# Kernel tuning notes

Hardware: AMD Instinct MI355X
Metric: run time of the kernel (lower is better)

## Reference

```python
import jax, jax.numpy as jnp
import numpy as np
import math

IN_DIM = 1024
INTER_DIM = 1024
HIDDEN_DIM = 1024
OUT_DIM = 1024
NUM_GROUPS = 16
N = 8192
EPS = 1e-5


def setup_inputs() -> dict:
    key = jax.random.key(0)
    ks = jax.random.split(key, 20)
    def lin(kw, kb, fan_out, fan_in):
        bound = 1.0 / math.sqrt(fan_in)
        W = jax.random.uniform(kw, (fan_out, fan_in), jnp.float32, -bound, bound)
        b = jax.random.uniform(kb, (fan_out,), jnp.float32, -bound, bound)
        return W, b
    Wq, bq = lin(ks[0], ks[1], INTER_DIM, IN_DIM)
    Wk, bk = lin(ks[2], ks[3], INTER_DIM, IN_DIM)
    Wv, bv = lin(ks[4], ks[5], INTER_DIM, IN_DIM)
    Wr, br = lin(ks[6], ks[7], HIDDEN_DIM, INTER_DIM)
    Wc, bc = lin(ks[8], ks[9], HIDDEN_DIM, OUT_DIM)
    Wp, bp = lin(ks[10], ks[11], OUT_DIM, 2 * HIDDEN_DIM)
    return {
        'h': jax.random.normal(ks[12], (N, IN_DIM), jnp.float32),
        'D': jax.random.uniform(ks[13], (N, N), jnp.float32),
        'h_prime': jax.random.normal(ks[14], (N, OUT_DIM), jnp.float32),
        'Wq': Wq, 'bq': bq, 'Wk': Wk, 'bk': bk, 'Wv': Wv, 'bv': bv,
        'Wr': Wr, 'br': br, 'Wc': Wc, 'bc': bc, 'Wp': Wp, 'bp': bp,
        'prelu_w': jnp.full((OUT_DIM,), 0.25, jnp.float32),
        'gn_w': jnp.ones((OUT_DIM,), jnp.float32),
        'gn_b': jnp.zeros((OUT_DIM,), jnp.float32),
    }


def reference(h, D, h_prime, Wq, bq, Wk, bk, Wv, bv, Wr, br, Wc, bc, Wp, bp, prelu_w, gn_w, gn_b):
    # projections [N, inter]
    Q = h @ Wq.T + bq
    K = h @ Wk.T + bk
    V = h @ Wv.T + bv
    # decay-masked retention: softmax(D * QK^T / sqrt(d)) @ V
    scores = (Q @ K.T) * (1.0 / math.sqrt(INTER_DIM))   # [N, N]
    attn = jax.nn.softmax(D * scores, axis=-1)
    h_ret = attn @ V                                     # [N, inter]
    h_ret = jax.nn.gelu(h_ret @ Wr.T + br, approximate=False)  # [N, hidden]
    h_cat = h_prime @ Wc.T + bc                          # [N, hidden]
    combined = jnp.concatenate([h_ret, h_cat], axis=-1)  # [N, 2*hidden]
    x = combined @ Wp.T + bp                             # [N, out]
    # PReLU (per-channel slope over feature dim)
    x = jnp.where(x >= 0, x, prelu_w[None, :] * x)
    # GroupNorm over (C, N) layout: normalize each group of channels jointly over all N
    xt = x.T                                             # [C, N]
    xg = xt.reshape(NUM_GROUPS, -1)                      # [G, (C/G)*N]
    mean = jnp.mean(xg, axis=1, keepdims=True)
    var = jnp.var(xg, axis=1, keepdims=True)
    xg = (xg - mean) * jax.lax.rsqrt(var + EPS)
    xt = xg.reshape(OUT_DIM, N) * gn_w[:, None] + gn_b[:, None]
    return xt.T                                          # [N, out]
```

## Files before the change

kernel.cpp:

```cpp
#include <hip/hip_runtime.h>
#include <hip/hip_bf16.h>


typedef __bf16 bf16x8 __attribute__((ext_vector_type(8)));
typedef float f32x4 __attribute__((ext_vector_type(4)));
typedef unsigned short ushort_t;
typedef unsigned short ushort8 __attribute__((ext_vector_type(8)));


__device__ __forceinline__ void gload_lds16(const void* g, void* lds) {
  __builtin_amdgcn_global_load_lds((const __attribute__((address_space(1))) void*)g,
                                   (__attribute__((address_space(3))) void*)lds,
                                   16, 0, 0);
}

__device__ __forceinline__ ushort_t f2bu(float x) {
  __hip_bfloat16 h = __float2bfloat16(x);
  return *reinterpret_cast<ushort_t*>(&h);
}

#define FENCE() asm volatile("" ::: "memory")
#define BARRIER() do { FENCE(); __builtin_amdgcn_s_barrier(); FENCE(); } while (0)


__global__ void f2b_kernel(const float* __restrict__ s, __hip_bfloat16* __restrict__ d, int n) {
  const int i4 = (blockIdx.x * 256 + threadIdx.x) * 4;
  if (i4 >= n) return;
  const float4 v = *(const float4*)(s + i4);
  ushort4 o;
  o.x = f2bu(v.x); o.y = f2bu(v.y); o.z = f2bu(v.z); o.w = f2bu(v.w);
  *(ushort4*)((ushort_t*)d + i4) = o;
}

template <int EPI>
__global__ __launch_bounds__(512, 2)
void g8(const __hip_bfloat16* __restrict__ A, const __hip_bfloat16* __restrict__ B,
        __hip_bfloat16* __restrict__ Cb, float* __restrict__ Cf,
        int K, int ldc, int nbnLog2,
        const float* __restrict__ biasN, const float* __restrict__ biasM,
        const float* __restrict__ rowsum, const float* __restrict__ prelu_w,
        float* __restrict__ gstats) {
  __shared__ __align__(16) char ldsm[98304];
  const int tid = threadIdx.x, w = tid >> 6, l = tid & 63;
  const int wm = w >> 2, wn = w & 3;

  const int orig = blockIdx.x;
  const int wg = (orig & 7) * 32 + (orig >> 3);
  const int bm = wg >> nbnLog2, bn = wg & ((1 << nbnLog2) - 1);

  const size_t rowB = (size_t)K * 2;
  const char* Ag = (const char*)A + (size_t)bm * 128 * rowB;
  const char* Bg = (const char*)B + (size_t)bn * 256 * rowB;
  const int NT = K >> 6;

  auto stageU = [&](int p, int unit, const char* srcbase) {
    char* ldsu = ldsm + p * 49152 + unit * 16384;
#pragma unroll
    for (int i = 0; i < 2; ++i) {
      const int cb = i * 512 + w * 64;
      const int c = cb + l;
      const int r = c >> 3;
      const int j = (c & 7) ^ (r & 7);
      gload_lds16(srcbase + (size_t)r * rowB + j * 16, ldsu + cb * 16);
    }
  };
  auto stA = [&](int p, int kt) { stageU(p, 0, Ag + (size_t)kt * 128); };
  auto stB = [&](int p, int hh, int kt) {
    stageU(p, 1 + hh, Bg + (size_t)hh * 128 * rowB + (size_t)kt * 128);
  };

  auto rdA = [&](int p, int f, int kk) -> bf16x8 {
    const int R = wm * 64 + f * 16 + (l & 15);
    const int j = kk * 4 + (l >> 4);
    const int chunk = R * 8 + (j ^ (R & 7));
    return *(const bf16x8*)(ldsm + p * 49152 + chunk * 16);
  };
  auto rdB = [&](int p, int nf, int kk) -> bf16x8 {
    const int Rg = wn * 64 + nf * 16 + (l & 15);
    const int hh = Rg >> 7, Rl = Rg & 127;
    const int j = kk * 4 + (l >> 4);
    const int chunk = Rl * 8 + (j ^ (Rl & 7));
    return *(const bf16x8*)(ldsm + p * 49152 + 16384 + hh * 16384 + chunk * 16);
  };

  stA(0, 0); stB(0, 0, 0); stB(0, 1, 0);
  stA(1, 1);
  asm volatile("s_waitcnt vmcnt(2)" ::: "memory");
  BARRIER();

  f32x4 acc[4][4] = {};
  bf16x8 Af[4][2], Bf[2][2];

#define PH_A_B01(p)                                            \
  _Pragma("unroll") for (int f = 0; f < 4; ++f)                \
  _Pragma("unroll") for (int kk = 0; kk < 2; ++kk)             \
      Af[f][kk] = rdA(p, f, kk);                               \
  _Pragma("unroll") for (int g = 0; g < 2; ++g)                \
  _Pragma("unroll") for (int kk = 0; kk < 2; ++kk)             \
      Bf[g][kk] = rdB(p, g, kk)

#define PH_B23(p)                                              \
  _Pragma("unroll") for (int g = 0; g < 2; ++g)                \
  _Pragma("unroll") for (int kk = 0; kk < 2; ++kk)             \
      Bf[g][kk] = rdB(p, 2 + g, kk)

#define PRE_MFMA()                                             \
  asm volatile("s_waitcnt lgkmcnt(0)" ::: "memory");           \
  __builtin_amdgcn_sched_barrier(0)

#define MF(CB)                                                          \
  __builtin_amdgcn_s_setprio(1);                                        \
  _Pragma("unroll") for (int kk = 0; kk < 2; ++kk)                      \
  _Pragma("unroll") for (int f = 0; f < 4; ++f)                         \
  _Pragma("unroll") for (int g = 0; g < 2; ++g)                         \
      acc[f][(CB) + g] = __builtin_amdgcn_mfma_f32_16x16x32_bf16(       \
          Af[f][kk], Bf[g][kk], acc[f][(CB) + g], 0, 0, 0);             \
  __builtin_amdgcn_s_setprio(0)

#pragma unroll 1
  for (int t = 0; t < NT; t += 2) {
    const bool s2 = (t + 2 < NT);
    PH_A_B01(0);
    stB(1, 0, t + 1); stB(1, 1, t + 1);
    BARRIER(); PRE_MFMA();
    MF(0);
    BARRIER();
    PH_B23(0);
    if (s2) stA(0, t + 2);
    if (s2) asm volatile("s_waitcnt vmcnt(2)" ::: "memory");
    else    asm volatile("s_waitcnt vmcnt(0)" ::: "memory");
    BARRIER(); PRE_MFMA();
    MF(2);
    BARRIER();
    PH_A_B01(1);
    if (s2) { stB(0, 0, t + 2); stB(0, 1, t + 2); }
    BARRIER(); PRE_MFMA();
    MF(0);
    BARRIER();
    PH_B23(1);
    if (s2) {
      stA(1, t + 3);
      asm volatile("s_waitcnt vmcnt(2)" ::: "memory");
    }
    BARRIER(); PRE_MFMA();
    MF(2);
    BARRIER();
  }
#undef PH_A_B01
#undef PH_B23
#undef PRE_MFMA
#undef MF

  const int r0 = bm * 128 + wm * 64, c0 = bn * 256 + wn * 64;
  float gs = 0.f, gq = 0.f;
#pragma unroll
  for (int mf = 0; mf < 4; ++mf) {
#pragma unroll
    for (int i = 0; i < 4; ++i) {
      const int row = r0 + mf * 16 + ((l >> 4) << 2) + i;
      float rscale = 1.0f;
      if (EPI == 3) rscale = 1.0f / rowsum[row];
#pragma unroll
      for (int nf = 0; nf < 4; ++nf) {
        const int col = c0 + nf * 16 + (l & 15);
        float v = acc[mf][nf][i];
        if (EPI == 0) {
          v += biasN[col];
        } else if (EPI == 1) {
          v += biasM[row];
        } else if (EPI == 3) {
          v = v * rscale + biasN[col];
          v = 0.5f * v * (1.0f + erff(v * 0.70710678118654752f));
        } else if (EPI == 4) {
          v += biasN[col];
          v = (v >= 0.f) ? v : prelu_w[col] * v;
        }
        if (EPI == 4) {
          Cf[(size_t)row * ldc + col] = v;
          gs += v; gq += v * v;
        } else {
          Cb[(size_t)row * ldc + col] = __float2bfloat16(v);
        }
      }
    }
  }
  if (EPI == 4) {
#pragma unroll
    for (int m = 1; m < 64; m <<= 1) {
      gs += __shfl_xor(gs, m);
      gq += __shfl_xor(gq, m);
    }
    if (l == 0) {
      const int g = c0 >> 6;
      atomicAdd(&gstats[g * 2 + 0], gs);
      atomicAdd(&gstats[g * 2 + 1], gq);
    }
  }
}

#define EPAD2 132
__global__ __launch_bounds__(256, 2)
void pkern2(const __hip_bfloat16* __restrict__ Q, const __hip_bfloat16* __restrict__ Kmat,
            const float* __restrict__ D, __hip_bfloat16* __restrict__ P,
            float* __restrict__ rowsum, int nt) {
  __shared__ __align__(16) char ldsm[65536];
  const int tid = threadIdx.x, w = tid >> 6, l = tid & 63;
  const int wm = w >> 1, wn = w & 1;

  const int orig = blockIdx.x;
  const int wg = (orig & 7) * 512 + (orig >> 3);
  const int bm = wg >> 6, bn = wg & 63;

  const char* Ag = (const char*)Q + (size_t)bm * 128 * 2048;
  const char* Bg = (const char*)Kmat + (size_t)bn * 128 * 2048;

  auto stageU = [&](int p, int unit, const char* srcbase) {
    char* ldsu = ldsm + p * 32768 + unit * 16384;
#pragma unroll
    for (int i = 0; i < 4; ++i) {
      const int cb = i * 256 + w * 64;
      const int c = cb + l;
      const int r = c >> 3;
      const int j = (c & 7) ^ (r & 7);
      gload_lds16(srcbase + (size_t)r * 2048 + j * 16, ldsu + cb * 16);
    }
  };
  auto stA = [&](int p, int kt) { stageU(p, 0, Ag + (size_t)kt * 128); };
  auto stB = [&](int p, int kt) { stageU(p, 1, Bg + (size_t)kt * 128); };

  auto rdA = [&](int p, int f, int kk) -> bf16x8 {
    const int R = wm * 64 + f * 16 + (l & 15);
    const int j = kk * 4 + (l >> 4);
    const int chunk = R * 8 + (j ^ (R & 7));
    return *(const bf16x8*)(ldsm + p * 32768 + chunk * 16);
  };
  auto rdB = [&](int p, int nf, int kk) -> bf16x8 {
    const int R = wn * 64 + nf * 16 + (l & 15);
    const int j = kk * 4 + (l >> 4);
    const int chunk = R * 8 + (j ^ (R & 7));
    return *(const bf16x8*)(ldsm + p * 32768 + 16384 + chunk * 16);
  };

  stA(0, 0); stB(0, 0);
  stA(1, 1);
  asm volatile("s_waitcnt vmcnt(4)" ::: "memory");
  BARRIER();

  f32x4 acc[4][4] = {};
  bf16x8 Af[4][2], Bf[2][2];

#define PH_A_B01(p)                                            \
  _Pragma("unroll") for (int f = 0; f < 4; ++f)                \
  _Pragma("unroll") for (int kk = 0; kk < 2; ++kk)             \
      Af[f][kk] = rdA(p, f, kk);                               \
  _Pragma("unroll") for (int g = 0; g < 2; ++g)                \
  _Pragma("unroll") for (int kk = 0; kk < 2; ++kk)             \
      Bf[g][kk] = rdB(p, g, kk)

#define PH_B23(p)                                              \
  _Pragma("unroll") for (int g = 0; g < 2; ++g)                \
  _Pragma("unroll") for (int kk = 0; kk < 2; ++kk)             \
      Bf[g][kk] = rdB(p, 2 + g, kk)

#define PRE_MFMA()                                             \
  asm volatile("s_waitcnt lgkmcnt(0)" ::: "memory");           \
  __builtin_amdgcn_sched_barrier(0)

#define MF(CB)                                                          \
  __builtin_amdgcn_s_setprio(1);                                        \
  _Pragma("unroll") for (int kk = 0; kk < 2; ++kk)                      \
  _Pragma("unroll") for (int f = 0; f < 4; ++f)                         \
  _Pragma("unroll") for (int g = 0; g < 2; ++g)                         \
      acc[f][(CB) + g] = __builtin_amdgcn_mfma_f32_16x16x32_bf16(       \
          Af[f][kk], Bf[g][kk], acc[f][(CB) + g], 0, 0, 0);             \
  __builtin_amdgcn_s_setprio(0)

#pragma unroll 1
  for (int t = 0; t < nt; t += 2) {
    const bool s2 = (t + 2 < nt), s3 = (t + 3 < nt);
    PH_A_B01(0);
    stB(1, t + 1);
    BARRIER(); PRE_MFMA();
    MF(0);
    BARRIER();
    PH_B23(0);
    if (s2) stA(0, t + 2);
    if (s2) asm volatile("s_waitcnt vmcnt(4)" ::: "memory");
    else    asm volatile("s_waitcnt vmcnt(0)" ::: "memory");
    BARRIER(); PRE_MFMA();
    MF(2);
    BARRIER();
    PH_A_B01(1);
    if (s2) stB(0, t + 2);
    BARRIER(); PRE_MFMA();
    MF(0);
    BARRIER();
    PH_B23(1);
    if (s3) stA(1, t + 3);
    if (s3)      asm volatile("s_waitcnt vmcnt(4)" ::: "memory");
    else if (s2) asm volatile("s_waitcnt vmcnt(0)" ::: "memory");
    else         asm volatile("s_waitcnt vmcnt(0)" ::: "memory");
    BARRIER(); PRE_MFMA();
    MF(2);
    BARRIER();
  }
#undef PH_A_B01
#undef PH_B23
#undef PRE_MFMA
#undef MF

  float* lds32 = (float*)ldsm;
  const int rbase = bm * 128, cbase = bn * 128;
  const int rth = tid >> 3;
  const int cl = (tid & 7) * 16;
#pragma unroll 1
  for (int h = 0; h < 2; ++h) {
    float4 dreg[8];
#pragma unroll
    for (int it = 0; it < 2; ++it) {
      const size_t gof = (size_t)(rbase + h * 64 + it * 32 + rth) * 8192 + (cbase + cl);
#pragma unroll
      for (int q = 0; q < 4; ++q) dreg[it * 4 + q] = *(const float4*)(D + gof + q * 4);
    }
    BARRIER();
    if (wm == h) {
#pragma unroll
      for (int mf = 0; mf < 4; ++mf)
#pragma unroll
        for (int nf = 0; nf < 4; ++nf)
#pragma unroll
          for (int i = 0; i < 4; ++i)
            lds32[(mf * 16 + ((l >> 4) << 2) + i) * EPAD2 + (wn * 64 + nf * 16 + (l & 15))] =
                acc[mf][nf][i];
    }
    asm volatile("s_waitcnt lgkmcnt(0)" ::: "memory");
    BARRIER();
#pragma unroll
    for (int it = 0; it < 2; ++it) {
      const int rl = it * 32 + rth;
      const int row = rbase + h * 64 + rl;
      const size_t gof = (size_t)row * 8192 + (cbase + cl);
      float pv[16];
#pragma unroll
      for (int q = 0; q < 4; ++q) {
        const float4 s = *(const float4*)(lds32 + rl * EPAD2 + cl + q * 4);
        const float4 d = dreg[it * 4 + q];
        pv[q * 4 + 0] = __expf(d.x * (s.x * 0.03125f));
        pv[q * 4 + 1] = __expf(d.y * (s.y * 0.03125f));
        pv[q * 4 + 2] = __expf(d.z * (s.z * 0.03125f));
        pv[q * 4 + 3] = __expf(d.w * (s.w * 0.03125f));
      }
      ushort8 o0, o1;
#pragma unroll
      for (int q = 0; q < 8; ++q) { o0[q] = f2bu(pv[q]); o1[q] = f2bu(pv[8 + q]); }
      *(ushort8*)((ushort_t*)P + gof) = o0;
      *(ushort8*)((ushort_t*)P + gof + 8) = o1;
      float rs = 0.f;
#pragma unroll
      for (int q = 0; q < 16; ++q) rs += pv[q];
      rs += __shfl_xor(rs, 1); rs += __shfl_xor(rs, 2); rs += __shfl_xor(rs, 4);
      if ((tid & 7) == 0) atomicAdd(&rowsum[row], rs);
    }
  }
}
#undef EPAD2


__global__ void gn_finalize(const float* __restrict__ x, const float* __restrict__ gstats,
                            const float* __restrict__ gw, const float* __restrict__ gb,
                            float* __restrict__ out, int n) {
  __shared__ float sm[16], sr[16];
  if (threadIdx.x < 16) {
    const float cnt = 64.0f * 8192.0f;
    const float s = gstats[threadIdx.x * 2 + 0];
    const float q = gstats[threadIdx.x * 2 + 1];
    const float mean = s / cnt;
    const float var = q / cnt - mean * mean;
    sm[threadIdx.x] = mean;
    sr[threadIdx.x] = rsqrtf(var + 1e-5f);
  }
  __syncthreads();
  const int i4 = (blockIdx.x * 256 + threadIdx.x) * 4;
  if (i4 >= n) return;
  const float4 v = *(const float4*)(x + i4);
  const int c = i4 & 1023;
  const int g = c >> 6;
  const float mean = sm[g], r = sr[g];
  float4 o;
  o.x = (v.x - mean) * r * gw[c + 0] + gb[c + 0];
  o.y = (v.y - mean) * r * gw[c + 1] + gb[c + 1];
  o.z = (v.z - mean) * r * gw[c + 2] + gb[c + 2];
  o.w = (v.w - mean) * r * gw[c + 3] + gb[c + 3];
  *(float4*)(out + i4) = o;
}


extern "C" void kernel_launch(void* const* d_in, const int* in_sizes, int n_in,
                              void* d_out, int out_size, void* d_ws, size_t ws_size,
                              hipStream_t stream) {
  const float* h  = (const float*)d_in[0];
  const float* D  = (const float*)d_in[1];
  const float* hp = (const float*)d_in[2];
  const float* Wq = (const float*)d_in[3];
  const float* bq = (const float*)d_in[4];
  const float* Wk = (const float*)d_in[5];
  const float* bk = (const float*)d_in[6];
  const float* Wv = (const float*)d_in[7];
  const float* bv = (const float*)d_in[8];
  const float* Wr = (const float*)d_in[9];
  const float* br = (const float*)d_in[10];
  const float* Wc = (const float*)d_in[11];
  const float* bc = (const float*)d_in[12];
  const float* Wp = (const float*)d_in[13];
  const float* bp = (const float*)d_in[14];
  const float* pw = (const float*)d_in[15];
  const float* gw = (const float*)d_in[16];
  const float* gb = (const float*)d_in[17];
  float* out = (float*)d_out;

  char* ws = (char*)d_ws;
  size_t off = 0;
  auto alloc = [&](size_t b) {
    char* p = ws + off;
    off += (b + 255) & ~(size_t)255;
    return p;
  };
  __hip_bfloat16* hb   = (__hip_bfloat16*)alloc(8192ull * 1024 * 2);
  __hip_bfloat16* hpb  = (__hip_bfloat16*)alloc(8192ull * 1024 * 2);
  __hip_bfloat16* Wqb  = (__hip_bfloat16*)alloc(1024ull * 1024 * 2);
  __hip_bfloat16* Wkb  = (__hip_bfloat16*)alloc(1024ull * 1024 * 2);
  __hip_bfloat16* Wvb  = (__hip_bfloat16*)alloc(1024ull * 1024 * 2);
  __hip_bfloat16* Wrb  = (__hip_bfloat16*)alloc(1024ull * 1024 * 2);
  __hip_bfloat16* Wcb  = (__hip_bfloat16*)alloc(1024ull * 1024 * 2);
  __hip_bfloat16* Wpb  = (__hip_bfloat16*)alloc(1024ull * 2048 * 2);
  __hip_bfloat16* Qb   = (__hip_bfloat16*)alloc(8192ull * 1024 * 2);
  __hip_bfloat16* Kb   = (__hip_bfloat16*)alloc(8192ull * 1024 * 2);
  __hip_bfloat16* Vt   = (__hip_bfloat16*)alloc(1024ull * 8192 * 2);
  __hip_bfloat16* R0   = (__hip_bfloat16*)alloc(8192ull * 1024 * 2);
  __hip_bfloat16* comb = (__hip_bfloat16*)alloc(8192ull * 2048 * 2);
  __hip_bfloat16* P    = (__hip_bfloat16*)alloc(8192ull * 8192 * 2);
  float* xbuf   = (float*)alloc(8192ull * 1024 * 4);
  float* rowsum = (float*)alloc(8192ull * 4);
  float* gstats = (float*)alloc(128);
  if (off > ws_size) return;

  hipMemsetAsync(rowsum, 0, 8192 * 4, stream);
  hipMemsetAsync(gstats, 0, 128, stream);

  auto cvt = [&](const float* s, __hip_bfloat16* d, int n) {
    f2b_kernel<<<dim3((n / 4 + 255) / 256), dim3(256), 0, stream>>>(s, d, n);
  };
  cvt(h, hb, 8192 * 1024);
  cvt(hp, hpb, 8192 * 1024);
  cvt(Wq, Wqb, 1024 * 1024);
  cvt(Wk, Wkb, 1024 * 1024);
  cvt(Wv, Wvb, 1024 * 1024);
  cvt(Wr, Wrb, 1024 * 1024);
  cvt(Wc, Wcb, 1024 * 1024);
  cvt(Wp, Wpb, 1024 * 2048);

  g8<0><<<dim3(256), 512, 0, stream>>>(hb, Wqb, Qb, nullptr, 1024, 1024, 2, bq, nullptr, nullptr, nullptr, nullptr);
  g8<0><<<dim3(256), 512, 0, stream>>>(hb, Wkb, Kb, nullptr, 1024, 1024, 2, bk, nullptr, nullptr, nullptr, nullptr);
  g8<1><<<dim3(256), 512, 0, stream>>>(Wvb, hb, Vt, nullptr, 1024, 8192, 5, nullptr, bv, nullptr, nullptr, nullptr);
  pkern2<<<dim3(4096), 256, 0, stream>>>(Qb, Kb, D, P, rowsum, 16);
  g8<2><<<dim3(256), 512, 0, stream>>>(P, Vt, R0, nullptr, 8192, 1024, 2, nullptr, nullptr, nullptr, nullptr, nullptr);
  g8<3><<<dim3(256), 512, 0, stream>>>(R0, Wrb, comb, nullptr, 1024, 2048, 2, br, nullptr, rowsum, nullptr, nullptr);
  g8<0><<<dim3(256), 512, 0, stream>>>(hpb, Wcb, comb + 1024, nullptr, 1024, 2048, 2, bc, nullptr, nullptr, nullptr, nullptr);
  g8<4><<<dim3(256), 512, 0, stream>>>(comb, Wpb, nullptr, xbuf, 2048, 1024, 2, bp, nullptr, nullptr, pw, gstats);
  gn_finalize<<<dim3(8192), 256, 0, stream>>>(xbuf, gstats, gw, gb, out, 8192 * 1024);
}
```

Baseline: 637.9 us.

## Triple-buffer GEMM pipeline, fuse fp32-to-bf16 conversions, retile score kernel blocks

Result: faster. 534.2 us (-16.3%).

```diff
diff --git a/kernel.cpp b/kernel.cpp
--- a/kernel.cpp
+++ b/kernel.cpp
@@ -23,24 +23,33 @@
 #define BARRIER() do { FENCE(); __builtin_amdgcn_s_barrier(); FENCE(); } while (0)
 
 
-__global__ void f2b_kernel(const float* __restrict__ s, __hip_bfloat16* __restrict__ d, int n) {
-  const int i4 = (blockIdx.x * 256 + threadIdx.x) * 4;
-  if (i4 >= n) return;
-  const float4 v = *(const float4*)(s + i4);
+struct CvtArgs {
+  const float* src[8];
+  __hip_bfloat16* dst[8];
+  int base[8];
+};
+
+__global__ void f2b_all(CvtArgs a) {
+  const int b = blockIdx.x;
+  int seg = 0;
+#pragma unroll
+  for (int s = 1; s < 8; ++s) seg = (b >= a.base[s]) ? s : seg;
+  const int i4 = (b - a.base[seg]) * 1024 + threadIdx.x * 4;
+  const float4 v = *(const float4*)(a.src[seg] + i4);
   ushort4 o;
   o.x = f2bu(v.x); o.y = f2bu(v.y); o.z = f2bu(v.z); o.w = f2bu(v.w);
-  *(ushort4*)((ushort_t*)d + i4) = o;
+  *(ushort4*)((ushort_t*)a.dst[seg] + i4) = o;
 }
 
 template <int EPI>
 __global__ __launch_bounds__(512, 2)
-void g8(const __hip_bfloat16* __restrict__ A, const __hip_bfloat16* __restrict__ B,
-        __hip_bfloat16* __restrict__ Cb, float* __restrict__ Cf,
-        int K, int ldc, int nbnLog2,
-        const float* __restrict__ biasN, const float* __restrict__ biasM,
-        const float* __restrict__ rowsum, const float* __restrict__ prelu_w,
-        float* __restrict__ gstats) {
-  __shared__ __align__(16) char ldsm[98304];
+void g1p(const __hip_bfloat16* __restrict__ A, const __hip_bfloat16* __restrict__ B,
+         __hip_bfloat16* __restrict__ Cb, float* __restrict__ Cf,
+         int K, int ldc, int nbnLog2,
+         const float* __restrict__ biasN, const float* __restrict__ biasM,
+         const float* __restrict__ rowsum, const float* __restrict__ prelu_w,
+         float* __restrict__ gstats) {
+  __shared__ __align__(16) char ldsm[147456];
   const int tid = threadIdx.x, w = tid >> 6, l = tid & 63;
   const int wm = w >> 2, wn = w & 3;
 
@@ -53,8 +62,7 @@
   const char* Bg = (const char*)B + (size_t)bn * 256 * rowB;
   const int NT = K >> 6;
 
-  auto stageU = [&](int p, int unit, const char* srcbase) {
-    char* ldsu = ldsm + p * 49152 + unit * 16384;
+  auto stageU = [&](char* ldsu, const char* srcbase) {
 #pragma unroll
     for (int i = 0; i < 2; ++i) {
       const int cb = i * 512 + w * 64;
@@ -64,92 +72,65 @@
       gload_lds16(srcbase + (size_t)r * rowB + j * 16, ldsu + cb * 16);
     }
   };
-  auto stA = [&](int p, int kt) { stageU(p, 0, Ag + (size_t)kt * 128); };
-  auto stB = [&](int p, int hh, int kt) {
-    stageU(p, 1 + hh, Bg + (size_t)hh * 128 * rowB + (size_t)kt * 128);
-  };
-
-  auto rdA = [&](int p, int f, int kk) -> bf16x8 {
+  auto stT = [&](char* buf, int kt) {
+    stageU(buf, Ag + (size_t)kt * 128);
+    stageU(buf + 16384, Bg + (size_t)kt * 128);
+    stageU(buf + 32768, Bg + (size_t)128 * rowB + (size_t)kt * 128);
+  };
+
+  auto rdA = [&](const char* buf, int f, int kk) -> bf16x8 {
     const int R = wm * 64 + f * 16 + (l & 15);
     const int j = kk * 4 + (l >> 4);
     const int chunk = R * 8 + (j ^ (R & 7));
-    return *(const bf16x8*)(ldsm + p * 49152 + chunk * 16);
-  };
-  auto rdB = [&](int p, int nf, int kk) -> bf16x8 {
+    return *(const bf16x8*)(buf + chunk * 16);
+  };
+  auto rdB = [&](const char* buf, int nf, int kk) -> bf16x8 {
     const int Rg = wn * 64 + nf * 16 + (l & 15);
     const int hh = Rg >> 7, Rl = Rg & 127;
     const int j = kk * 4 + (l >> 4);
     const int chunk = Rl * 8 + (j ^ (Rl & 7));
-    return *(const bf16x8*)(ldsm + p * 49152 + 16384 + hh * 16384 + chunk * 16);
-  };
-
-  stA(0, 0); stB(0, 0, 0); stB(0, 1, 0);
-  stA(1, 1);
-  asm volatile("s_waitcnt vmcnt(2)" ::: "memory");
+    return *(const bf16x8*)(buf + 16384 + hh * 16384 + chunk * 16);
+  };
+
+  char* pa = ldsm;
+  char* pb = ldsm + 49152;
+  char* pc = ldsm + 98304;
+
+  stT(pa, 0); stT(pb, 1);
+  asm volatile("s_waitcnt vmcnt(6)" ::: "memory");
   BARRIER();
 
   f32x4 acc[4][4] = {};
-  bf16x8 Af[4][2], Bf[2][2];
-
-#define PH_A_B01(p)                                            \
-  _Pragma("unroll") for (int f = 0; f < 4; ++f)                \
-  _Pragma("unroll") for (int kk = 0; kk < 2; ++kk)             \
-      Af[f][kk] = rdA(p, f, kk);                               \
-  _Pragma("unroll") for (int g = 0; g < 2; ++g)                \
-  _Pragma("unroll") for (int kk = 0; kk < 2; ++kk)             \
-      Bf[g][kk] = rdB(p, g, kk)
-
-#define PH_B23(p)                                              \
-  _Pragma("unroll") for (int g = 0; g < 2; ++g)                \
-  _Pragma("unroll") for (int kk = 0; kk < 2; ++kk)             \
-      Bf[g][kk] = rdB(p, 2 + g, kk)
-
-#define PRE_MFMA()                                             \
-  asm volatile("s_waitcnt lgkmcnt(0)" ::: "memory");           \
-  __builtin_amdgcn_sched_barrier(0)
-
-#define MF(CB)                                                          \
-  __builtin_amdgcn_s_setprio(1);                                        \
-  _Pragma("unroll") for (int kk = 0; kk < 2; ++kk)                      \
-  _Pragma("unroll") for (int f = 0; f < 4; ++f)                         \
-  _Pragma("unroll") for (int g = 0; g < 2; ++g)                         \
-      acc[f][(CB) + g] = __builtin_amdgcn_mfma_f32_16x16x32_bf16(       \
-          Af[f][kk], Bf[g][kk], acc[f][(CB) + g], 0, 0, 0);             \
-  __builtin_amdgcn_s_setprio(0)
+  bf16x8 Af[4][2], Bf[4][2];
 
 #pragma unroll 1
-  for (int t = 0; t < NT; t += 2) {
-    const bool s2 = (t + 2 < NT);
-    PH_A_B01(0);
-    stB(1, 0, t + 1); stB(1, 1, t + 1);
-    BARRIER(); PRE_MFMA();
-    MF(0);
-    BARRIER();
-    PH_B23(0);
-    if (s2) stA(0, t + 2);
-    if (s2) asm volatile("s_waitcnt vmcnt(2)" ::: "memory");
-    else    asm volatile("s_waitcnt vmcnt(0)" ::: "memory");
-    BARRIER(); PRE_MFMA();
-    MF(2);
-    BARRIER();
-    PH_A_B01(1);
-    if (s2) { stB(0, 0, t + 2); stB(0, 1, t + 2); }
-    BARRIER(); PRE_MFMA();
-    MF(0);
-    BARRIER();
-    PH_B23(1);
-    if (s2) {
-      stA(1, t + 3);
-      asm volatile("s_waitcnt vmcnt(2)" ::: "memory");
-    }
-    BARRIER(); PRE_MFMA();
-    MF(2);
-    BARRIER();
-  }
-#undef PH_A_B01
-#undef PH_B23
-#undef PRE_MFMA
-#undef MF
+  for (int t = 0; t < NT; ++t) {
+    const bool s1 = (t + 1 < NT), s2 = (t + 2 < NT);
+#pragma unroll
+    for (int f = 0; f < 4; ++f)
+#pragma unroll
+      for (int kk = 0; kk < 2; ++kk) Af[f][kk] = rdA(pa, f, kk);
+#pragma unroll
+    for (int nf = 0; nf < 4; ++nf)
+#pragma unroll
+      for (int kk = 0; kk < 2; ++kk) Bf[nf][kk] = rdB(pa, nf, kk);
+    if (s2) stT(pc, t + 2);
+    asm volatile("s_waitcnt lgkmcnt(0)" ::: "memory");
+    __builtin_amdgcn_sched_barrier(0);
+    __builtin_amdgcn_s_setprio(1);
+#pragma unroll
+    for (int kk = 0; kk < 2; ++kk)
+#pragma unroll
+      for (int f = 0; f < 4; ++f)
+#pragma unroll
+        for (int g = 0; g < 4; ++g)
+          acc[f][g] = __builtin_amdgcn_mfma_f32_16x16x32_bf16(Af[f][kk], Bf[g][kk], acc[f][g], 0, 0, 0);
+    __builtin_amdgcn_s_setprio(0);
+    if (s2)      asm volatile("s_waitcnt vmcnt(6)" ::: "memory");
+    else if (s1) asm volatile("s_waitcnt vmcnt(0)" ::: "memory");
+    BARRIER();
+    char* tmp = pa; pa = pb; pb = pc; pc = tmp;
+  }
 
   const int r0 = bm * 128 + wm * 64, c0 = bn * 256 + wn * 64;
   float gs = 0.f, gq = 0.f;
@@ -200,45 +181,49 @@
 
 #define EPAD2 132
 __global__ __launch_bounds__(256, 2)
-void pkern2(const __hip_bfloat16* __restrict__ Q, const __hip_bfloat16* __restrict__ Kmat,
-            const float* __restrict__ D, __hip_bfloat16* __restrict__ P,
-            float* __restrict__ rowsum, int nt) {
+void pkern2s(const __hip_bfloat16* __restrict__ Q, const __hip_bfloat16* __restrict__ Kmat,
+             const float* __restrict__ D, __hip_bfloat16* __restrict__ P,
+             float* __restrict__ rowsum, int nt) {
   __shared__ __align__(16) char ldsm[65536];
   const int tid = threadIdx.x, w = tid >> 6, l = tid & 63;
   const int wm = w >> 1, wn = w & 1;
 
   const int orig = blockIdx.x;
-  const int wg = (orig & 7) * 512 + (orig >> 3);
-  const int bm = wg >> 6, bn = wg & 63;
+  const int x = orig & 7;
+  const int i = orig >> 3;
+  const int sr = i >> 6;
+  const int p = i & 63;
+  const int bm = sr * 8 + (p >> 3);
+  const int bn = x * 8 + (p & 7);
 
   const char* Ag = (const char*)Q + (size_t)bm * 128 * 2048;
   const char* Bg = (const char*)Kmat + (size_t)bn * 128 * 2048;
 
-  auto stageU = [&](int p, int unit, const char* srcbase) {
-    char* ldsu = ldsm + p * 32768 + unit * 16384;
-#pragma unroll
-    for (int i = 0; i < 4; ++i) {
-      const int cb = i * 256 + w * 64;
+  auto stageU = [&](int pbuf, int unit, const char* srcbase) {
+    char* ldsu = ldsm + pbuf * 32768 + unit * 16384;
+#pragma unroll
+    for (int q = 0; q < 4; ++q) {
+      const int cb = q * 256 + w * 64;
       const int c = cb + l;
       const int r = c >> 3;
       const int j = (c & 7) ^ (r & 7);
       gload_lds16(srcbase + (size_t)r * 2048 + j * 16, ldsu + cb * 16);
     }
   };
-  auto stA = [&](int p, int kt) { stageU(p, 0, Ag + (size_t)kt * 128); };
-  auto stB = [&](int p, int kt) { stageU(p, 1, Bg + (size_t)kt * 128); };
-
-  auto rdA = [&](int p, int f, int kk) -> bf16x8 {
+  auto stA = [&](int pbuf, int kt) { stageU(pbuf, 0, Ag + (size_t)kt * 128); };
+  auto stB = [&](int pbuf, int kt) { stageU(pbuf, 1, Bg + (size_t)kt * 128); };
+
+  auto rdA = [&](int pbuf, int f, int kk) -> bf16x8 {
     const int R = wm * 64 + f * 16 + (l & 15);
     const int j = kk * 4 + (l >> 4);
     const int chunk = R * 8 + (j ^ (R & 7));
-    return *(const bf16x8*)(ldsm + p * 32768 + chunk * 16);
-  };
-  auto rdB = [&](int p, int nf, int kk) -> bf16x8 {
+    return *(const bf16x8*)(ldsm + pbuf * 32768 + chunk * 16);
+  };
+  auto rdB = [&](int pbuf, int nf, int kk) -> bf16x8 {
     const int R = wn * 64 + nf * 16 + (l & 15);
     const int j = kk * 4 + (l >> 4);
     const int chunk = R * 8 + (j ^ (R & 7));
-    return *(const bf16x8*)(ldsm + p * 32768 + 16384 + chunk * 16);
+    return *(const bf16x8*)(ldsm + pbuf * 32768 + 16384 + chunk * 16);
   };
 
   stA(0, 0); stB(0, 0);
@@ -249,18 +234,18 @@
   f32x4 acc[4][4] = {};
   bf16x8 Af[4][2], Bf[2][2];
 
-#define PH_A_B01(p)                                            \
+#define PH_A_B01(pbuf)                                         \
   _Pragma("unroll") for (int f = 0; f < 4; ++f)                \
   _Pragma("unroll") for (int kk = 0; kk < 2; ++kk)             \
-      Af[f][kk] = rdA(p, f, kk);                               \
+      Af[f][kk] = rdA(pbuf, f, kk);                            \
   _Pragma("unroll") for (int g = 0; g < 2; ++g)                \
   _Pragma("unroll") for (int kk = 0; kk < 2; ++kk)             \
-      Bf[g][kk] = rdB(p, g, kk)
-
-#define PH_B23(p)                                              \
+      Bf[g][kk] = rdB(pbuf, g, kk)
+
+#define PH_B23(pbuf)                                           \
   _Pragma("unroll") for (int g = 0; g < 2; ++g)                \
   _Pragma("unroll") for (int kk = 0; kk < 2; ++kk)             \
-      Bf[g][kk] = rdB(p, 2 + g, kk)
+      Bf[g][kk] = rdB(pbuf, 2 + g, kk)
 
 #define PRE_MFMA()                                             \
   asm volatile("s_waitcnt lgkmcnt(0)" ::: "memory");           \
@@ -329,9 +314,9 @@
 #pragma unroll
         for (int nf = 0; nf < 4; ++nf)
 #pragma unroll
-          for (int i = 0; i < 4; ++i)
-            lds32[(mf * 16 + ((l >> 4) << 2) + i) * EPAD2 + (wn * 64 + nf * 16 + (l & 15))] =
-                acc[mf][nf][i];
+          for (int i2 = 0; i2 < 4; ++i2)
+            lds32[(mf * 16 + ((l >> 4) << 2) + i2) * EPAD2 + (wn * 64 + nf * 16 + (l & 15))] =
+                acc[mf][nf][i2];
     }
     asm volatile("s_waitcnt lgkmcnt(0)" ::: "memory");
     BARRIER();
@@ -447,25 +432,24 @@
   hipMemsetAsync(rowsum, 0, 8192 * 4, stream);
   hipMemsetAsync(gstats, 0, 128, stream);
 
-  auto cvt = [&](const float* s, __hip_bfloat16* d, int n) {
-    f2b_kernel<<<dim3((n / 4 + 255) / 256), dim3(256), 0, stream>>>(s, d, n);
-  };
-  cvt(h, hb, 8192 * 1024);
-  cvt(hp, hpb, 8192 * 1024);
-  cvt(Wq, Wqb, 1024 * 1024);
-  cvt(Wk, Wkb, 1024 * 1024);
-  cvt(Wv, Wvb, 1024 * 1024);
-  cvt(Wr, Wrb, 1024 * 1024);
-  cvt(Wc, Wcb, 1024 * 1024);
-  cvt(Wp, Wpb, 1024 * 2048);
-
-  g8<0><<<dim3(256), 512, 0, stream>>>(hb, Wqb, Qb, nullptr, 1024, 1024, 2, bq, nullptr, nullptr, nullptr, nullptr);
-  g8<0><<<dim3(256), 512, 0, stream>>>(hb, Wkb, Kb, nullptr, 1024, 1024, 2, bk, nullptr, nullptr, nullptr, nullptr);
-  g8<1><<<dim3(256), 512, 0, stream>>>(Wvb, hb, Vt, nullptr, 1024, 8192, 5, nullptr, bv, nullptr, nullptr, nullptr);
-  pkern2<<<dim3(4096), 256, 0, stream>>>(Qb, Kb, D, P, rowsum, 16);
-  g8<2><<<dim3(256), 512, 0, stream>>>(P, Vt, R0, nullptr, 8192, 1024, 2, nullptr, nullptr, nullptr, nullptr, nullptr);
-  g8<3><<<dim3(256), 512, 0, stream>>>(R0, Wrb, comb, nullptr, 1024, 2048, 2, br, nullptr, rowsum, nullptr, nullptr);
-  g8<0><<<dim3(256), 512, 0, stream>>>(hpb, Wcb, comb + 1024, nullptr, 1024, 2048, 2, bc, nullptr, nullptr, nullptr, nullptr);
-  g8<4><<<dim3(256), 512, 0, stream>>>(comb, Wpb, nullptr, xbuf, 2048, 1024, 2, bp, nullptr, nullptr, pw, gstats);
+  CvtArgs ca;
+  ca.src[0] = h;  ca.dst[0] = hb;  ca.base[0] = 0;
+  ca.src[1] = hp; ca.dst[1] = hpb; ca.base[1] = 8192;
+  ca.src[2] = Wq; ca.dst[2] = Wqb; ca.base[2] = 16384;
+  ca.src[3] = Wk; ca.dst[3] = Wkb; ca.base[3] = 17408;
+  ca.src[4] = Wv; ca.dst[4] = Wvb; ca.base[4] = 18432;
+  ca.src[5] = Wr; ca.dst[5] = Wrb; ca.base[5] = 19456;
+  ca.src[6] = Wc; ca.dst[6] = Wcb; ca.base[6] = 20480;
+  ca.src[7] = Wp; ca.dst[7] = Wpb; ca.base[7] = 21504;
+  f2b_all<<<dim3(23552), 256, 0, stream>>>(ca);
+
+  g1p<0><<<dim3(256), 512, 0, stream>>>(hb, Wqb, Qb, nullptr, 1024, 1024, 2, bq, nullptr, nullptr, nullptr, nullptr);
+  g1p<0><<<dim3(256), 512, 0, stream>>>(hb, Wkb, Kb, nullptr, 1024, 1024, 2, bk, nullptr, nullptr, nullptr, nullptr);
+  g1p<1><<<dim3(256), 512, 0, stream>>>(Wvb, hb, Vt, nullptr, 1024, 8192, 5, nullptr, bv, nullptr, nullptr, nullptr);
+  pkern2s<<<dim3(4096), 256, 0, stream>>>(Qb, Kb, D, P, rowsum, 16);
+  g1p<2><<<dim3(256), 512, 0, stream>>>(P, Vt, R0, nullptr, 8192, 1024, 2, nullptr, nullptr, nullptr, nullptr, nullptr);
+  g1p<3><<<dim3(256), 512, 0, stream>>>(R0, Wrb, comb, nullptr, 1024, 2048, 2, br, nullptr, rowsum, nullptr, nullptr);
+  g1p<0><<<dim3(256), 512, 0, stream>>>(hpb, Wcb, comb + 1024, nullptr, 1024, 2048, 2, bc, nullptr, nullptr, nullptr, nullptr);
+  g1p<4><<<dim3(256), 512, 0, stream>>>(comb, Wpb, nullptr, xbuf, 2048, 1024, 2, bp, nullptr, nullptr, pw, gstats);
   gn_finalize<<<dim3(8192), 256, 0, stream>>>(xbuf, gstats, gw, gb, out, 8192 * 1024);
 }
```
